# Performance work log

Hardware: AMD Instinct MI355X
Metric: run time of the kernel (lower is better)

## Reference

```python
import jax, jax.numpy as jnp
import numpy as np

B, N, DN = 8, 4096, 64
E = 1048576
H, DM = 128, 64   # message MLP: 2*DN -> H -> DM
HU, F = 128, 64   # node-update MLP: DN+DM -> HU -> F


def setup_inputs() -> dict:
    key = jax.random.key(0)
    ks = jax.random.split(key, 13)
    inp = {
        'node_feats': jax.random.normal(ks[0], (B, N, DN), dtype=jnp.float32),
        'edge_b': jax.random.randint(ks[1], (E,), 0, B, dtype=jnp.int32),
        'edge_src': jax.random.randint(ks[2], (E,), 0, N, dtype=jnp.int32),
        'edge_dst': jax.random.randint(ks[3], (E,), 0, N, dtype=jnp.int32),
        'edge_vals': jax.random.uniform(ks[4], (E,), dtype=jnp.float32),
        # message MLP params (Dense-relu, Dense-linear)
        'Wm1': jax.random.normal(ks[5], (2 * DN, H), dtype=jnp.float32) / np.sqrt(2 * DN),
        'bm1': jnp.zeros((H,), jnp.float32),
        'Wm2': jax.random.normal(ks[6], (H, DM), dtype=jnp.float32) / np.sqrt(H),
        'bm2': jnp.zeros((DM,), jnp.float32),
        # node-update MLP params
        'Wu1': jax.random.normal(ks[7], (DN + DM, HU), dtype=jnp.float32) / np.sqrt(DN + DM),
        'bu1': jnp.zeros((HU,), jnp.float32),
        'Wu2': jax.random.normal(ks[8], (HU, F), dtype=jnp.float32) / np.sqrt(HU),
        'bu2': jnp.zeros((F,), jnp.float32),
    }
    return inp


def reference(node_feats, edge_b, edge_src, edge_dst, edge_vals,
              Wm1, bm1, Wm2, bm2, Wu1, bu1, Wu2, bu2):
    # --- create messages: gather src/target feats per edge ---
    src_feats = node_feats[edge_b, edge_src]            # (E, DN)
    tgt_feats = node_feats[edge_b, edge_dst]            # (E, DN)
    feats = jnp.concatenate([src_feats, tgt_feats], axis=-1)  # (E, 2*DN)
    h = jax.nn.relu(feats @ Wm1 + bm1)
    messages = h @ Wm2 + bm2                            # (E, DM)

    # --- gather (scatter) messages: weighted ragged segment-mean ---
    weighted = messages * edge_vals[:, None]            # (E, DM)
    seg = edge_b * N + edge_src                          # rowids b*max_N + src
    sums = jax.ops.segment_sum(weighted, seg, num_segments=B * N)
    counts = jax.ops.segment_sum(jnp.ones((E,), weighted.dtype), seg,
                                 num_segments=B * N)
    gathered = sums / jnp.maximum(counts, 1.0)[:, None]  # mean; 0 for empty rows
    gathered = gathered.reshape(B, N, DM)

    # --- update nodes ---
    upd_in = jnp.concatenate([node_feats, gathered], axis=-1)  # (B, N, DN+DM)
    hu = jax.nn.relu(upd_in @ Wu1 + bu1)
    updated = hu @ Wu2 + bu2                            # (B, N, F)
    return updated
```

## Files before the change

### kernel.cpp

```cpp
#include <hip/hip_runtime.h>

#define NB 8
#define NN 4096
#define DNF 64
#define NEDGE 1048576
#define DM 64
#define FF 64

#define NBKT2 2048
#define SPB2 16
#define NXCD 8
#define SUBCAP 192
#define OVFCAP 65536

using f32x4 = __attribute__((ext_vector_type(4))) float;
using s16x8 = __attribute__((ext_vector_type(8))) short;

__device__ __forceinline__ unsigned short f2b(float f) {
    union { float f; unsigned u; } v; v.f = f;
    unsigned r = (v.u + 0x7fffu + ((v.u >> 16) & 1u)) >> 16;
    return (unsigned short)r;
}
__device__ __forceinline__ float uif(unsigned u) {
    union { unsigned u; float f; } v; v.u = u;
    return v.f;
}

__device__ __forceinline__ void pack_one(const float* __restrict__ W,
                                         unsigned short* __restrict__ out,
                                         int K, int Ncols, int idx) {
    int j = idx & 7;
    int lane = (idx >> 3) & 63;
    int frag = idx >> 9;
    int KS = K >> 5;
    int ks = frag % KS;
    int nt = frag / KS;
    int k = ks * 32 + ((lane >> 4) << 3) + j;
    int col = nt * 16 + (lane & 15);
    out[idx] = f2b(W[k * Ncols + col]);
}

__global__ void pack_all(const float* __restrict__ Wm1, const float* __restrict__ Wm2,
                         const float* __restrict__ Wu1, const float* __restrict__ Wu2,
                         unsigned short* __restrict__ Qw, unsigned short* __restrict__ Pw,
                         unsigned short* __restrict__ Wm2p,
                         unsigned short* __restrict__ Wu1p, unsigned short* __restrict__ Wu2p) {
    int idx = blockIdx.x * 256 + threadIdx.x;
    if (idx < 8192)        pack_one(Wm1,              Qw,   64, 128, idx);
    else if (idx < 16384)  pack_one(Wm1 + 64 * 128,   Pw,   64, 128, idx - 8192);
    else if (idx < 24576)  pack_one(Wm2,              Wm2p, 128, 64, idx - 16384);
    else if (idx < 40960)  pack_one(Wu1,              Wu1p, 128, 128, idx - 24576);
    else                   pack_one(Wu2,              Wu2p, 128, 64, idx - 40960);
}

__global__ void pack_weights(const float* __restrict__ W, unsigned short* __restrict__ out,
                             int K, int Ncols) {
    int idx = blockIdx.x * 256 + threadIdx.x;
    if (idx >= K * Ncols) return;
    pack_one(W, out, K, Ncols, idx);
}

__launch_bounds__(256, 4)
__global__ void precompute_pq(const float* __restrict__ X,
                              const unsigned short* __restrict__ Qw,
                              const unsigned short* __restrict__ Pw,
                              const float* __restrict__ b1,
                              unsigned short* __restrict__ Qp,
                              unsigned short* __restrict__ Pp) {
    __shared__ unsigned short A[64][72];
    const int tid = threadIdx.x;
    const int g0 = blockIdx.x * 64;
    for (int i = 0; i < 16; ++i) {
        int idx = i * 256 + tid;
        int node = idx >> 6;
        int f = idx & 63;
        A[node][f] = f2b(X[(size_t)(g0 + node) * DNF + f]);
    }
    __syncthreads();
    const int wave = tid >> 6, lane = tid & 63;
    const int lr = lane & 15, lq = lane >> 4;
    const int arow = wave * 16 + lr;
    s16x8 a[2];
#pragma unroll
    for (int ks = 0; ks < 2; ++ks)
        a[ks] = *reinterpret_cast<const s16x8*>(&A[arow][ks * 32 + lq * 8]);
#pragma unroll
    for (int nt = 0; nt < 8; ++nt) {
        f32x4 accQ = {0.f, 0.f, 0.f, 0.f};
        f32x4 accP = {0.f, 0.f, 0.f, 0.f};
#pragma unroll
        for (int ks = 0; ks < 2; ++ks) {
            s16x8 bq = *reinterpret_cast<const s16x8*>(&Qw[(((nt << 1) + ks) * 64 + lane) * 8]);
            s16x8 bp = *reinterpret_cast<const s16x8*>(&Pw[(((nt << 1) + ks) * 64 + lane) * 8]);
            accQ = __builtin_amdgcn_mfma_f32_16x16x32_bf16(a[ks], bq, accQ, 0, 0, 0);
            accP = __builtin_amdgcn_mfma_f32_16x16x32_bf16(a[ks], bp, accP, 0, 0, 0);
        }
        int col = nt * 16 + lr;
        float bias = b1[col];
#pragma unroll
        for (int j = 0; j < 4; ++j) {
            int row = g0 + wave * 16 + lq * 4 + j;
            Qp[(size_t)row * 128 + col] = f2b(accQ[j] + bias);
            Pp[(size_t)row * 128 + col] = f2b(accP[j]);
        }
    }
}

__launch_bounds__(256, 8)
__global__ void scatter_xcd(const int* __restrict__ eb, const int* __restrict__ esrc,
                            const int* __restrict__ edst, const float* __restrict__ evals,
                            unsigned* __restrict__ gcurX, unsigned* __restrict__ payslot,
                            unsigned* __restrict__ ovf_cnt, unsigned* __restrict__ ovf_seg,
                            unsigned* __restrict__ ovf_pay) {
    unsigned xcd;
    asm volatile("s_getreg_b32 %0, hwreg(HW_REG_XCC_ID)" : "=s"(xcd));
    xcd &= (NXCD - 1);
    const int t0 = blockIdx.x * 1024 + threadIdx.x;
    int seg[4]; unsigned pk[4];
#pragma unroll
    for (int k = 0; k < 4; ++k) {
        int e = t0 + k * 256;
        seg[k] = eb[e] * NN + esrc[e];
        unsigned wq = (unsigned)fminf(evals[e] * 8192.0f + 0.5f, 8191.0f);
        pk[k] = (unsigned)edst[e] | (wq << 12) | ((unsigned)(seg[k] & 15) << 25);
    }
    unsigned pos[4];
#pragma unroll
    for (int k = 0; k < 4; ++k)
        pos[k] = atomicAdd(&gcurX[xcd * NBKT2 + (seg[k] >> 4)], 1u);
#pragma unroll
    for (int k = 0; k < 4; ++k) {
        if (pos[k] < (unsigned)SUBCAP) {
            payslot[((size_t)(seg[k] >> 4) * NXCD + xcd) * SUBCAP + pos[k]] = pk[k];
        } else {
            unsigned o = atomicAdd(ovf_cnt, 1u);
            if (o < (unsigned)OVFCAP) { ovf_seg[o] = (unsigned)seg[k]; ovf_pay[o] = pk[k]; }
        }
    }
}

__launch_bounds__(256, 6)
__global__ void bucket16_fused(const unsigned short* __restrict__ Qp,
                               const unsigned short* __restrict__ Pp,
                               const unsigned* __restrict__ payslot,
                               const unsigned* __restrict__ gcurX,
                               const unsigned* __restrict__ ovf_cnt,
                               const unsigned* __restrict__ ovf_seg,
                               const unsigned* __restrict__ ovf_pay,
                               const unsigned short* __restrict__ Wm2p,
                               const float* __restrict__ b2m,
                               const float* __restrict__ X,
                               const unsigned short* __restrict__ Wu1p,
                               const float* __restrict__ bu1,
                               const unsigned short* __restrict__ Wu2p,
                               const float* __restrict__ bu2,
                               float* __restrict__ out) {
    __shared__ unsigned raw[NXCD * SUBCAP];
    __shared__ unsigned sorted[NXCD * SUBCAP];
    __shared__ unsigned short S[16][136];
    __shared__ unsigned short A1[16][136];
    __shared__ unsigned short Hs[16][136];
    __shared__ unsigned h4[4][16];
    __shared__ unsigned offs[17];
    __shared__ unsigned curb[16];
    __shared__ unsigned cx[NXCD];
    __shared__ float SW[16], SC[16];
    const int tid = threadIdx.x, wv = tid >> 6, lane = tid & 63;
    const int bkt = (blockIdx.x & 7) * 256 + (blockIdx.x >> 3);
    const int node0 = bkt * SPB2;
    const int rowbase = (bkt >> 8) << 12;
    const unsigned novf = ovf_cnt[0];

#pragma unroll
    for (int i = 0; i < 4; ++i) {
        int idx = i * 256 + tid;
        int row = idx >> 6, f = idx & 63;
        A1[row][f] = f2b(X[(size_t)(node0 + row) * DNF + f]);
    }
    if (tid < 64) ((unsigned*)h4)[tid] = 0;
    if (tid < NXCD) cx[tid] = min(gcurX[tid * NBKT2 + bkt], (unsigned)SUBCAP);
    __syncthreads();
    for (int x = 0; x < NXCD; ++x) {
        unsigned c = cx[x];
        for (unsigned i = tid; i < c; i += 256) {
            unsigned v = payslot[((size_t)bkt * NXCD + x) * SUBCAP + i];
            raw[x * SUBCAP + i] = v;
            atomicAdd(&h4[wv][(v >> 25) & 15u], 1u);
        }
    }
    __syncthreads();
    if (tid < 16) {
        int xx = (int)(h4[0][tid] + h4[1][tid] + h4[2][tid] + h4[3][tid]);
#pragma unroll
        for (int o = 1; o < 16; o <<= 1) {
            int y = __shfl_up(xx, o);
            if (tid >= o) xx += y;
        }
        offs[tid + 1] = (unsigned)xx;
        if (tid == 0) offs[0] = 0;
    }
    __syncthreads();
    if (tid < 16) curb[tid] = offs[tid];
    __syncthreads();
    for (int x = 0; x < NXCD; ++x) {
        unsigned c = cx[x];
        for (unsigned i = tid; i < c; i += 256) {
            unsigned v = raw[x * SUBCAP + i];
            unsigned pos = atomicAdd(&curb[(v >> 25) & 15u], 1u);
            sorted[pos] = v;
        }
    }
    __syncthreads();

    const unsigned* P32 = reinterpret_cast<const unsigned*>(Pp);
    const unsigned* Q32 = reinterpret_cast<const unsigned*>(Qp);
    const unsigned* Pb = P32 + (size_t)rowbase * 64 + lane;
    for (int si = 0; si < 4; ++si) {
        const int lo = wv * 4 + si;
        const int seg = node0 + lo;
        const unsigned s0 = offs[lo], s1 = offs[lo + 1];
        unsigned qv = Q32[(size_t)seg * 64 + lane];
        float q0 = uif(qv << 16);
        float q1 = uif(qv & 0xffff0000u);
        float acc0 = 0.f, acc1 = 0.f, wsum = 0.f;
        unsigned scnt = s1 - s0;

        for (unsigned bse = s0; bse < s1; bse += 8) {
            unsigned pv[8]; float wf[8];
#pragma unroll
            for (int k = 0; k < 8; ++k) {
                unsigned idx = bse + (unsigned)k;
                unsigned c = (idx < s1) ? sorted[idx] : 0u;
                wf[k] = (float)((c >> 12) & 8191u) * (1.0f / 8192.0f);
                pv[k] = Pb[(size_t)(c & 0xfffu) * 64];
            }
#pragma unroll
            for (int k = 0; k < 8; ++k) {
                float p0 = uif(pv[k] << 16);
                float p1 = uif(pv[k] & 0xffff0000u);
                acc0 = fmaf(wf[k], fmaxf(q0 + p0, 0.f), acc0);
                acc1 = fmaf(wf[k], fmaxf(q1 + p1, 0.f), acc1);
                wsum += wf[k];
            }
        }
        if (novf > 0) {
            unsigned ncl = min(novf, (unsigned)OVFCAP);
            for (unsigned i = 0; i < ncl; ++i) {
                if (ovf_seg[i] == (unsigned)seg) {
                    unsigned c = ovf_pay[i];
                    float w = (float)((c >> 12) & 8191u) * (1.0f / 8192.0f);
                    unsigned pv = Pb[(size_t)(c & 0xfffu) * 64];
                    acc0 = fmaf(w, fmaxf(q0 + uif(pv << 16), 0.f), acc0);
                    acc1 = fmaf(w, fmaxf(q1 + uif(pv & 0xffff0000u), 0.f), acc1);
                    wsum += w;
                    scnt += 1;
                }
            }
        }
        unsigned sp = (unsigned)f2b(acc0) | ((unsigned)f2b(acc1) << 16);
        *reinterpret_cast<unsigned*>(&S[lo][2 * lane]) = sp;
        if (lane == 0) {
            SW[lo] = wsum;
            SC[lo] = 1.0f / (float)max(scnt, 1u);
        }
    }
    __syncthreads();

    const int lr = lane & 15, lq = lane >> 4;
    {
        s16x8 a[4];
#pragma unroll
        for (int ks = 0; ks < 4; ++ks)
            a[ks] = *reinterpret_cast<const s16x8*>(&S[lr][ks * 32 + lq * 8]);
        f32x4 acc = {0.f, 0.f, 0.f, 0.f};
#pragma unroll
        for (int ks = 0; ks < 4; ++ks) {
            s16x8 bf = *reinterpret_cast<const s16x8*>(&Wm2p[(((wv << 2) + ks) * 64 + lane) * 8]);
            acc = __builtin_amdgcn_mfma_f32_16x16x32_bf16(a[ks], bf, acc, 0, 0, 0);
        }
        float bb = b2m[wv * 16 + lr];
#pragma unroll
        for (int j = 0; j < 4; ++j) {
            int r = lq * 4 + j;
            float g = (acc[j] + SW[r] * bb) * SC[r];
            A1[r][64 + wv * 16 + lr] = f2b(g);
        }
    }
    __syncthreads();

    {
        s16x8 a1[4];
#pragma unroll
        for (int ks = 0; ks < 4; ++ks)
            a1[ks] = *reinterpret_cast<const s16x8*>(&A1[lr][ks * 32 + lq * 8]);
#pragma unroll
        for (int t = 0; t < 2; ++t) {
            int nt = wv * 2 + t;
            f32x4 acc = {0.f, 0.f, 0.f, 0.f};
#pragma unroll
            for (int ks = 0; ks < 4; ++ks) {
                s16x8 bf = *reinterpret_cast<const s16x8*>(&Wu1p[(((nt << 2) + ks) * 64 + lane) * 8]);
                acc = __builtin_amdgcn_mfma_f32_16x16x32_bf16(a1[ks], bf, acc, 0, 0, 0);
            }
            float bias = bu1[nt * 16 + lr];
#pragma unroll
            for (int j = 0; j < 4; ++j) {
                float hh = fmaxf(acc[j] + bias, 0.f);
                Hs[lq * 4 + j][nt * 16 + lr] = f2b(hh);
            }
        }
    }
    __syncthreads();

    {
        s16x8 a2[4];
#pragma unroll
        for (int ks = 0; ks < 4; ++ks)
            a2[ks] = *reinterpret_cast<const s16x8*>(&Hs[lr][ks * 32 + lq * 8]);
        f32x4 acc = {0.f, 0.f, 0.f, 0.f};
#pragma unroll
        for (int ks = 0; ks < 4; ++ks) {
            s16x8 bf = *reinterpret_cast<const s16x8*>(&Wu2p[(((wv << 2) + ks) * 64 + lane) * 8]);
            acc = __builtin_amdgcn_mfma_f32_16x16x32_bf16(a2[ks], bf, acc, 0, 0, 0);
        }
        float bias = bu2[wv * 16 + lr];
#pragma unroll
        for (int j = 0; j < 4; ++j)
            out[(size_t)(node0 + lq * 4 + j) * FF + wv * 16 + lr] = acc[j] + bias;
    }
}


template<int SCALE>
__launch_bounds__(256, 4)
__global__ void node_kernel(const float* __restrict__ node_feats,
                            const float* __restrict__ sums, const float* __restrict__ counts,
                            const unsigned short* __restrict__ W1p, const float* __restrict__ b1,
                            const unsigned short* __restrict__ W2p, const float* __restrict__ b2,
                            float* __restrict__ out) {
    __shared__ unsigned short A1[64][136];
    __shared__ unsigned short Hs[64][136];
    const int tid = threadIdx.x;
    const int g0 = blockIdx.x * 64;
    for (int i = 0; i < 16; ++i) {
        int idx = i * 256 + tid;
        int node = idx >> 6;
        int p = idx & 63;
        int g = g0 + node;
        float2 v;
        if (p < 32) {
            v = *reinterpret_cast<const float2*>(node_feats + (size_t)g * DNF + 2 * p);
        } else {
            float2 s = *reinterpret_cast<const float2*>(sums + (size_t)g * DM + 2 * p - 64);
            if (SCALE) {
                float scale = 1.0f / fmaxf(counts[g], 1.0f);
                s.x *= scale; s.y *= scale;
            }
            v = s;
        }
        unsigned packed = (unsigned)f2b(v.x) | ((unsigned)f2b(v.y) << 16);
        *reinterpret_cast<unsigned*>(&A1[node][2 * p]) = packed;
    }
    __syncthreads();
    const int wave = tid >> 6, lane = tid & 63;
    const int lr = lane & 15, lq = lane >> 4;
    const int arow = wave * 16 + lr;
    s16x8 a[4];
#pragma unroll
    for (int ks = 0; ks < 4; ++ks)
        a[ks] = *reinterpret_cast<const s16x8*>(&A1[arow][ks * 32 + lq * 8]);
#pragma unroll
    for (int nt = 0; nt < 8; ++nt) {
        f32x4 acc = {0.f, 0.f, 0.f, 0.f};
#pragma unroll
        for (int ks = 0; ks < 4; ++ks) {
            s16x8 bf = *reinterpret_cast<const s16x8*>(&W1p[(((nt << 2) + ks) * 64 + lane) * 8]);
            acc = __builtin_amdgcn_mfma_f32_16x16x32_bf16(a[ks], bf, acc, 0, 0, 0);
        }
        float bias = b1[nt * 16 + lr];
#pragma unroll
        for (int j = 0; j < 4; ++j) {
            float h = acc[j] + bias;
            h = h > 0.f ? h : 0.f;
            Hs[wave * 16 + lq * 4 + j][nt * 16 + lr] = f2b(h);
        }
    }
    s16x8 a2[4];
#pragma unroll
    for (int ks = 0; ks < 4; ++ks)
        a2[ks] = *reinterpret_cast<const s16x8*>(&Hs[arow][ks * 32 + lq * 8]);
#pragma unroll
    for (int nt = 0; nt < 4; ++nt) {
        f32x4 acc = {0.f, 0.f, 0.f, 0.f};
#pragma unroll
        for (int ks = 0; ks < 4; ++ks) {
            s16x8 bf = *reinterpret_cast<const s16x8*>(&W2p[(((nt << 2) + ks) * 64 + lane) * 8]);
            acc = __builtin_amdgcn_mfma_f32_16x16x32_bf16(a2[ks], bf, acc, 0, 0, 0);
        }
        float bias = b2[nt * 16 + lr];
#pragma unroll
        for (int j = 0; j < 4; ++j) {
            int g = g0 + wave * 16 + lq * 4 + j;
            out[(size_t)g * FF + nt * 16 + lr] = acc[j] + bias;
        }
    }
}

__launch_bounds__(256, 4)
__global__ void edge_kernel(const float* __restrict__ node_feats,
                            const int* __restrict__ eb, const int* __restrict__ esrc,
                            const int* __restrict__ edst, const float* __restrict__ evals,
                            const unsigned short* __restrict__ W1p, const float* __restrict__ b1,
                            const unsigned short* __restrict__ W2p, const float* __restrict__ b2,
                            float* __restrict__ sums, float* __restrict__ counts) {
    __shared__ unsigned short A1[64][136];
    __shared__ unsigned short Hs[64][136];
    const int tid = threadIdx.x;
    const int e0 = blockIdx.x * 64;
    if (tid < 64) {
        int e = e0 + tid;
        atomicAdd(&counts[eb[e] * NN + esrc[e]], 1.0f);
    }
    for (int i = 0; i < 16; ++i) {
        int idx = i * 256 + tid;
        int edge = idx >> 6;
        int p = idx & 63;
        int e = e0 + edge;
        int b = eb[e];
        const float* row;
        if (p < 32) row = node_feats + ((size_t)b * NN + esrc[e]) * DNF;
        else        row = node_feats + ((size_t)b * NN + edst[e]) * DNF - 64;
        float2 v = *reinterpret_cast<const float2*>(row + 2 * p);
        unsigned packed = (unsigned)f2b(v.x) | ((unsigned)f2b(v.y) << 16);
        *reinterpret_cast<unsigned*>(&A1[edge][2 * p]) = packed;
    }
    __syncthreads();
    const int wave = tid >> 6, lane = tid & 63;
    const int lr = lane & 15, lq = lane >> 4;
    const int arow = wave * 16 + lr;
    s16x8 a[4];
#pragma unroll
    for (int ks = 0; ks < 4; ++ks)
        a[ks] = *reinterpret_cast<const s16x8*>(&A1[arow][ks * 32 + lq * 8]);
#pragma unroll
    for (int nt = 0; nt < 8; ++nt) {
        f32x4 acc = {0.f, 0.f, 0.f, 0.f};
#pragma unroll
        for (int ks = 0; ks < 4; ++ks) {
            s16x8 bf = *reinterpret_cast<const s16x8*>(&W1p[(((nt << 2) + ks) * 64 + lane) * 8]);
            acc = __builtin_amdgcn_mfma_f32_16x16x32_bf16(a[ks], bf, acc, 0, 0, 0);
        }
        float bias = b1[nt * 16 + lr];
#pragma unroll
        for (int j = 0; j < 4; ++j) {
            float h = acc[j] + bias;
            h = h > 0.f ? h : 0.f;
            Hs[wave * 16 + lq * 4 + j][nt * 16 + lr] = f2b(h);
        }
    }
    s16x8 a2[4];
#pragma unroll
    for (int ks = 0; ks < 4; ++ks)
        a2[ks] = *reinterpret_cast<const s16x8*>(&Hs[arow][ks * 32 + lq * 8]);
    float ev[4]; int seg4[4];
#pragma unroll
    for (int j = 0; j < 4; ++j) {
        int r = e0 + wave * 16 + lq * 4 + j;
        ev[j] = evals[r];
        seg4[j] = eb[r] * NN + esrc[r];
    }
#pragma unroll
    for (int nt = 0; nt < 4; ++nt) {
        f32x4 acc = {0.f, 0.f, 0.f, 0.f};
#pragma unroll
        for (int ks = 0; ks < 4; ++ks) {
            s16x8 bf = *reinterpret_cast<const s16x8*>(&W2p[(((nt << 2) + ks) * 64 + lane) * 8]);
            acc = __builtin_amdgcn_mfma_f32_16x16x32_bf16(a2[ks], bf, acc, 0, 0, 0);
        }
        float bias = b2[nt * 16 + lr];
#pragma unroll
        for (int j = 0; j < 4; ++j) {
            float m = (acc[j] + bias) * ev[j];
            atomicAdd(&sums[(size_t)seg4[j] * DM + nt * 16 + lr], m);
        }
    }
}

extern "C" void kernel_launch(void* const* d_in, const int* in_sizes, int n_in,
                              void* d_out, int out_size, void* d_ws, size_t ws_size,
                              hipStream_t stream) {
    const float* node_feats = (const float*)d_in[0];
    const int*   eb    = (const int*)d_in[1];
    const int*   esrc  = (const int*)d_in[2];
    const int*   edst  = (const int*)d_in[3];
    const float* evals = (const float*)d_in[4];
    const float* Wm1 = (const float*)d_in[5];
    const float* bm1 = (const float*)d_in[6];
    const float* Wm2 = (const float*)d_in[7];
    const float* bm2 = (const float*)d_in[8];
    const float* Wu1 = (const float*)d_in[9];
    const float* bu1 = (const float*)d_in[10];
    const float* Wu2 = (const float*)d_in[11];
    const float* bu2 = (const float*)d_in[12];
    float* out = (float*)d_out;
    char* ws = (char*)d_ws;

    const size_t NEED = 30048384;
    if (ws_size >= NEED) {
        unsigned short* Qp      = (unsigned short*)(ws);
        unsigned short* Pp      = (unsigned short*)(ws + 8388608);
        unsigned*       payslot = (unsigned*)(ws + 16777216);
        unsigned*       gcurX   = (unsigned*)(ws + 29360128);
        unsigned*       ovf_cnt = (unsigned*)(ws + 29425664);
        unsigned*       ovf_seg = (unsigned*)(ws + 29425792);
        unsigned*       ovf_pay = (unsigned*)(ws + 29687936);
        unsigned short* Qw      = (unsigned short*)(ws + 29950080);
        unsigned short* Pw      = (unsigned short*)(ws + 29966464);
        unsigned short* Wu1p    = (unsigned short*)(ws + 29982848);
        unsigned short* Wu2p    = (unsigned short*)(ws + 30015616);
        unsigned short* Wm2p    = (unsigned short*)(ws + 30032000);

        hipMemsetAsync(gcurX, 0, 65536 + 128, stream);
        pack_all<<<192, 256, 0, stream>>>(Wm1, Wm2, Wu1, Wu2, Qw, Pw, Wm2p, Wu1p, Wu2p);
        precompute_pq<<<512, 256, 0, stream>>>(node_feats, Qw, Pw, bm1, Qp, Pp);
        scatter_xcd<<<NEDGE / 1024, 256, 0, stream>>>(eb, esrc, edst, evals,
                                                      gcurX, payslot, ovf_cnt, ovf_seg, ovf_pay);
        bucket16_fused<<<NBKT2, 256, 0, stream>>>(Qp, Pp, payslot, gcurX,
                                                  ovf_cnt, ovf_seg, ovf_pay,
                                                  Wm2p, bm2, node_feats,
                                                  Wu1p, bu1, Wu2p, bu2, out);
    } else {
        float* counts          = (float*)ws;
        unsigned short* W1p    = (unsigned short*)(ws + 131072);
        unsigned short* W2p    = (unsigned short*)(ws + 163840);
        unsigned short* Wu1p   = (unsigned short*)(ws + 180224);
        unsigned short* Wu2p   = (unsigned short*)(ws + 212992);
        hipMemsetAsync(d_out, 0, (size_t)out_size * sizeof(float), stream);
        hipMemsetAsync(counts, 0, 32768 * sizeof(float), stream);
        pack_weights<<<64, 256, 0, stream>>>(Wm1, W1p, 128, 128);
        pack_weights<<<32, 256, 0, stream>>>(Wm2, W2p, 128, 64);
        pack_weights<<<64, 256, 0, stream>>>(Wu1, Wu1p, 128, 128);
        pack_weights<<<32, 256, 0, stream>>>(Wu2, Wu2p, 128, 64);
        edge_kernel<<<NEDGE / 64, 256, 0, stream>>>(node_feats, eb, esrc, edst, evals,
                                                    W1p, bm1, W2p, bm2, out, counts);
        node_kernel<1><<<(NB * NN) / 64, 256, 0, stream>>>(node_feats, out, counts,
                                                           Wu1p, bu1, Wu2p, bu2, out);
    }
}
```

Measured before the change: 120.0 us.

## Pad bucket counters per cache line and use per-wave sort cursors

```diff
diff --git a/kernel.cpp b/kernel.cpp
--- a/kernel.cpp
+++ b/kernel.cpp
@@ -10,8 +10,8 @@
 #define NBKT2 2048
 #define SPB2 16
 #define NXCD 8
-#define SUBCAP 192
-#define OVFCAP 65536
+#define SUBCAP 176
+#define OVFCAP 32768
 
 using f32x4 = __attribute__((ext_vector_type(4))) float;
 using s16x8 = __attribute__((ext_vector_type(8))) short;
@@ -109,7 +109,7 @@
 __launch_bounds__(256, 8)
 __global__ void scatter_xcd(const int* __restrict__ eb, const int* __restrict__ esrc,
                             const int* __restrict__ edst, const float* __restrict__ evals,
-                            unsigned* __restrict__ gcurX, unsigned* __restrict__ payslot,
+                            unsigned* __restrict__ gcurP, unsigned* __restrict__ payslot,
                             unsigned* __restrict__ ovf_cnt, unsigned* __restrict__ ovf_seg,
                             unsigned* __restrict__ ovf_pay) {
     unsigned xcd;
@@ -127,7 +127,7 @@
     unsigned pos[4];
 #pragma unroll
     for (int k = 0; k < 4; ++k)
-        pos[k] = atomicAdd(&gcurX[xcd * NBKT2 + (seg[k] >> 4)], 1u);
+        pos[k] = atomicAdd(&gcurP[(xcd * NBKT2 + (seg[k] >> 4)) * 16], 1u);
 #pragma unroll
     for (int k = 0; k < 4; ++k) {
         if (pos[k] < (unsigned)SUBCAP) {
@@ -143,7 +143,7 @@
 __global__ void bucket16_fused(const unsigned short* __restrict__ Qp,
                                const unsigned short* __restrict__ Pp,
                                const unsigned* __restrict__ payslot,
-                               const unsigned* __restrict__ gcurX,
+                               const unsigned* __restrict__ gcurP,
                                const unsigned* __restrict__ ovf_cnt,
                                const unsigned* __restrict__ ovf_seg,
                                const unsigned* __restrict__ ovf_pay,
@@ -161,8 +161,8 @@
     __shared__ unsigned short A1[16][136];
     __shared__ unsigned short Hs[16][136];
     __shared__ unsigned h4[4][16];
+    __shared__ unsigned curb4[4][16];
     __shared__ unsigned offs[17];
-    __shared__ unsigned curb[16];
     __shared__ unsigned cx[NXCD];
     __shared__ float SW[16], SC[16];
     const int tid = threadIdx.x, wv = tid >> 6, lane = tid & 63;
@@ -178,11 +178,13 @@
         A1[row][f] = f2b(X[(size_t)(node0 + row) * DNF + f]);
     }
     if (tid < 64) ((unsigned*)h4)[tid] = 0;
-    if (tid < NXCD) cx[tid] = min(gcurX[tid * NBKT2 + bkt], (unsigned)SUBCAP);
-    __syncthreads();
-    for (int x = 0; x < NXCD; ++x) {
+    if (tid < NXCD) cx[tid] = min(gcurP[(tid * NBKT2 + bkt) * 16], (unsigned)SUBCAP);
+    __syncthreads();
+#pragma unroll
+    for (int xi = 0; xi < 2; ++xi) {
+        int x = wv * 2 + xi;
         unsigned c = cx[x];
-        for (unsigned i = tid; i < c; i += 256) {
+        for (unsigned i = lane; i < c; i += 64) {
             unsigned v = payslot[((size_t)bkt * NXCD + x) * SUBCAP + i];
             raw[x * SUBCAP + i] = v;
             atomicAdd(&h4[wv][(v >> 25) & 15u], 1u);
@@ -200,13 +202,20 @@
         if (tid == 0) offs[0] = 0;
     }
     __syncthreads();
-    if (tid < 16) curb[tid] = offs[tid];
-    __syncthreads();
-    for (int x = 0; x < NXCD; ++x) {
+    if (tid < 64) {
+        int w = tid >> 4, b = tid & 15;
+        unsigned base = offs[b];
+        for (int w2 = 0; w2 < w; ++w2) base += h4[w2][b];
+        curb4[w][b] = base;
+    }
+    __syncthreads();
+#pragma unroll
+    for (int xi = 0; xi < 2; ++xi) {
+        int x = wv * 2 + xi;
         unsigned c = cx[x];
-        for (unsigned i = tid; i < c; i += 256) {
+        for (unsigned i = lane; i < c; i += 64) {
             unsigned v = raw[x * SUBCAP + i];
-            unsigned pos = atomicAdd(&curb[(v >> 25) & 15u], 1u);
+            unsigned pos = atomicAdd(&curb4[wv][(v >> 25) & 15u], 1u);
             sorted[pos] = v;
         }
     }
@@ -222,8 +231,14 @@
         unsigned qv = Q32[(size_t)seg * 64 + lane];
         float q0 = uif(qv << 16);
         float q1 = uif(qv & 0xffff0000u);
-        float acc0 = 0.f, acc1 = 0.f, wsum = 0.f;
+        float acc0 = 0.f, acc1 = 0.f;
         unsigned scnt = s1 - s0;
+
+        float wl = 0.f;
+        for (unsigned i = s0 + lane; i < s1; i += 64)
+            wl += (float)((sorted[i] >> 12) & 8191u);
+        for (int m2 = 1; m2 < 64; m2 <<= 1) wl += __shfl_xor(wl, m2);
+        float wsum = wl * (1.0f / 8192.0f);
 
         for (unsigned bse = s0; bse < s1; bse += 8) {
             unsigned pv[8]; float wf[8];
@@ -240,7 +255,6 @@
                 float p1 = uif(pv[k] & 0xffff0000u);
                 acc0 = fmaf(wf[k], fmaxf(q0 + p0, 0.f), acc0);
                 acc1 = fmaf(wf[k], fmaxf(q1 + p1, 0.f), acc1);
-                wsum += wf[k];
             }
         }
         if (novf > 0) {
@@ -505,27 +519,27 @@
     float* out = (float*)d_out;
     char* ws = (char*)d_ws;
 
-    const size_t NEED = 30048384;
+    const size_t NEED = 29720704;
     if (ws_size >= NEED) {
         unsigned short* Qp      = (unsigned short*)(ws);
         unsigned short* Pp      = (unsigned short*)(ws + 8388608);
         unsigned*       payslot = (unsigned*)(ws + 16777216);
-        unsigned*       gcurX   = (unsigned*)(ws + 29360128);
-        unsigned*       ovf_cnt = (unsigned*)(ws + 29425664);
-        unsigned*       ovf_seg = (unsigned*)(ws + 29425792);
-        unsigned*       ovf_pay = (unsigned*)(ws + 29687936);
-        unsigned short* Qw      = (unsigned short*)(ws + 29950080);
-        unsigned short* Pw      = (unsigned short*)(ws + 29966464);
-        unsigned short* Wu1p    = (unsigned short*)(ws + 29982848);
-        unsigned short* Wu2p    = (unsigned short*)(ws + 30015616);
-        unsigned short* Wm2p    = (unsigned short*)(ws + 30032000);
-
-        hipMemsetAsync(gcurX, 0, 65536 + 128, stream);
+        unsigned*       gcurP   = (unsigned*)(ws + 28311552);
+        unsigned*       ovf_cnt = (unsigned*)(ws + 29360128);
+        unsigned*       ovf_seg = (unsigned*)(ws + 29360256);
+        unsigned*       ovf_pay = (unsigned*)(ws + 29491328);
+        unsigned short* Qw      = (unsigned short*)(ws + 29622400);
+        unsigned short* Pw      = (unsigned short*)(ws + 29638784);
+        unsigned short* Wu1p    = (unsigned short*)(ws + 29655168);
+        unsigned short* Wu2p    = (unsigned short*)(ws + 29687936);
+        unsigned short* Wm2p    = (unsigned short*)(ws + 29704320);
+
+        hipMemsetAsync(gcurP, 0, 1048576 + 128, stream);
         pack_all<<<192, 256, 0, stream>>>(Wm1, Wm2, Wu1, Wu2, Qw, Pw, Wm2p, Wu1p, Wu2p);
         precompute_pq<<<512, 256, 0, stream>>>(node_feats, Qw, Pw, bm1, Qp, Pp);
         scatter_xcd<<<NEDGE / 1024, 256, 0, stream>>>(eb, esrc, edst, evals,
-                                                      gcurX, payslot, ovf_cnt, ovf_seg, ovf_pay);
-        bucket16_fused<<<NBKT2, 256, 0, stream>>>(Qp, Pp, payslot, gcurX,
+                                                      gcurP, payslot, ovf_cnt, ovf_seg, ovf_pay);
+        bucket16_fused<<<NBKT2, 256, 0, stream>>>(Qp, Pp, payslot, gcurP,
                                                   ovf_cnt, ovf_seg, ovf_pay,
                                                   Wm2p, bm2, node_feats,
                                                   Wu1p, bu1, Wu2p, bu2, out);
```

Result: no change. 118.9 us (-0.9%).
